# Kernel tuning notes

Hardware: AMD Instinct MI355X
Metric: run time of the kernel (lower is better)

Reference implementation:

```python
import jax, jax.numpy as jnp
import numpy as np

N, E, D_IN, D_HID, D_OUT = 100000, 1200000, 64, 64, 32


def setup_inputs() -> dict:
    key = jax.random.key(0)
    ks = jax.random.split(key, 8)
    x = jax.random.normal(ks[0], (N, D_IN), dtype=jnp.float32)
    edge_index = jax.random.randint(ks[1], (2, E), 0, N, dtype=jnp.int64)

    def w(k, din, dout):
        return jax.random.normal(k, (din, dout), dtype=jnp.float32) / jnp.sqrt(jnp.float32(din))

    return {
        "x": x,
        "edge_index": edge_index,
        # SAGEConv layer 1: lin_l (on aggregated neighbors, with bias) + lin_r (on self, no bias)
        "W_l1": w(ks[2], D_IN, D_HID),
        "W_r1": w(ks[3], D_IN, D_HID),
        "b1": jnp.zeros((D_HID,), jnp.float32),
        # SAGEConv layer 2
        "W_l2": w(ks[4], D_HID, D_OUT),
        "W_r2": w(ks[5], D_HID, D_OUT),
        "b2": jnp.zeros((D_OUT,), jnp.float32),
    }


def _sage_conv(x, src, dst, W_l, W_r, b, n_nodes):
    # mean-aggregate source features into destination nodes (PyG default 'mean')
    summed = jax.ops.segment_sum(x[src], dst, num_segments=n_nodes)          # [N, D]
    deg = jax.ops.segment_sum(jnp.ones(src.shape, x.dtype), dst, num_segments=n_nodes)
    mean = summed / jnp.maximum(deg, 1.0)[:, None]
    # out = lin_l(mean_neighbors) + lin_r(self)
    return mean @ W_l + b + x @ W_r


def reference(x, edge_index, W_l1, W_r1, b1, W_l2, W_r2, b2):
    src, dst = edge_index[0], edge_index[1]
    n_nodes = x.shape[0]
    h = _sage_conv(x, src, dst, W_l1, W_r1, b1, n_nodes)
    h = jax.nn.relu(h)
    out = _sage_conv(h, src, dst, W_l2, W_r2, b2, n_nodes)
    return out
```

## Files before the change

### kernel.cpp

```cpp
#include <hip/hip_runtime.h>
#include <hip/hip_bf16.h>


#define CHUNK 2048
#define BSHIFT 7
#define BCAP  2048

typedef __attribute__((ext_vector_type(8))) short bf8;
typedef __attribute__((ext_vector_type(4))) float f4;

__device__ __forceinline__ unsigned short f2b(float f) {
    unsigned u = __float_as_uint(f);
    u += 0x7FFF + ((u >> 16) & 1);
    return (unsigned short)(u >> 16);
}

__device__ __forceinline__ bf8 load8f(const float* __restrict__ p) {
    float4 u0 = *(const float4*)p, u1 = *(const float4*)(p + 4);
    bf8 r;
    r[0] = (short)f2b(u0.x); r[1] = (short)f2b(u0.y);
    r[2] = (short)f2b(u0.z); r[3] = (short)f2b(u0.w);
    r[4] = (short)f2b(u1.x); r[5] = (short)f2b(u1.y);
    r[6] = (short)f2b(u1.z); r[7] = (short)f2b(u1.w);
    return r;
}

__device__ __forceinline__ int edge_src(const int* ei, int E, int e, bool i64) {
    return i64 ? ei[2 * e] : ei[e];
}
__device__ __forceinline__ int edge_dst(const int* ei, int E, int e, bool i64) {
    return i64 ? ei[2 * E + 2 * e] : ei[E + e];
}

__global__ __launch_bounds__(256) void prep(
        const float* __restrict__ Wl1, const float* __restrict__ Wr1,
        const float* __restrict__ Wl2, const float* __restrict__ Wr2,
        const int* __restrict__ ei,
        unsigned short* __restrict__ Bp1, unsigned short* __restrict__ Bp2,
        int* __restrict__ flag, int* __restrict__ gcursor, int nbuck) {
    int blk = blockIdx.x, t = threadIdx.x;
    if (blk < 32) {
        int idx = blk * 256 + t;
        int j = idx & 7, lane = (idx >> 3) & 63, ks = (idx >> 9) & 1, ct = idx >> 10;
        int k = ks * 32 + ((lane >> 4) << 3) + j;
        int c = ct * 16 + (lane & 15);
        float v = (c < 64) ? Wl1[k * 64 + c] : Wr1[k * 64 + (c - 64)];
        Bp1[idx] = f2b(v);
    } else if (blk < 48) {
        int e = (blk - 32) * 256 + t;
        int j = e & 7, lane = (e >> 3) & 63, ks = (e >> 9) & 1, ct = e >> 10;
        int k = ks * 32 + ((lane >> 4) << 3) + j;
        int c = ct * 16 + (lane & 15);
        float v = (c < 32) ? Wl2[k * 32 + c] : Wr2[k * 32 + (c - 32)];
        Bp2[e] = f2b(v);
    } else {
        if (t == 0) *flag = 0;
        __syncthreads();
        int v = ei[2 * t + 1];
        if (v != 0) atomicOr(flag, 1);
        for (int b = t; b < nbuck; b += 256) gcursor[b] = b * BCAP;
    }
}

__global__ __launch_bounds__(256) void k_scatter(
        const int* __restrict__ ei, int E, const int* __restrict__ flag,
        int* __restrict__ gcursor, int* __restrict__ bucketed, int nbuck) {
    __shared__ int lhist[1024];
    __shared__ int wgbase[1024];
    int t = threadIdx.x;
#pragma unroll
    for (int i = 0; i < 4; ++i) lhist[t + 256 * i] = 0;
    __syncthreads();
    bool i64 = (flag[0] == 0);
    int base = blockIdx.x * CHUNK;
    int p[CHUNK / 256];
    int bk[CHUNK / 256];
#pragma unroll
    for (int i = 0; i < CHUNK / 256; ++i) {
        int e = base + i * 256 + t;
        if (e < E) {
            int s = edge_src(ei, E, e, i64);
            int d = edge_dst(ei, E, e, i64);
            p[i] = s | ((d & 127) << 24);
            bk[i] = d >> BSHIFT;
            atomicAdd(&lhist[bk[i]], 1);
        } else {
            bk[i] = -1;
        }
    }
    __syncthreads();
    for (int b = t; b < nbuck; b += 256) {
        int c = lhist[b];
        wgbase[b] = c ? atomicAdd(&gcursor[b], c) : 0;
        lhist[b] = 0;
    }
    __syncthreads();
#pragma unroll
    for (int i = 0; i < CHUNK / 256; ++i) {
        if (bk[i] >= 0) {
            int r = atomicAdd(&lhist[bk[i]], 1);
            bucketed[wgbase[bk[i]] + r] = p[i];
        }
    }
}

__global__ __launch_bounds__(256) void k_bfinal(
        const int* __restrict__ bucketed, const int* __restrict__ gcursor,
        int* __restrict__ rs, int* __restrict__ re,
        int* __restrict__ adj, int n) {
    __shared__ int ledge[BCAP];
    __shared__ unsigned short lrank[BCAP];
    __shared__ int ldeg[128];
    __shared__ int lstart[257];
    int t = threadIdx.x, b = blockIdx.x;
    int start = b * BCAP;
    int cnt = gcursor[b] - start;
    if (cnt > BCAP) cnt = BCAP;
    for (int i = t; i < cnt; i += 256) ledge[i] = bucketed[start + i];
    if (t < 128) ldeg[t] = 0;
    __syncthreads();
    for (int i = t; i < cnt; i += 256) {
        int dl = ((unsigned)ledge[i]) >> 24;
        lrank[i] = (unsigned short)atomicAdd(&ldeg[dl], 1);
    }
    __syncthreads();
    int v = (t < 128) ? ldeg[t] : 0;
    lstart[t + 1] = v;
    if (t == 0) lstart[0] = 0;
    __syncthreads();
    for (int off = 1; off < 256; off <<= 1) {
        int add = (t + 1 > off) ? lstart[t + 1 - off] : 0;
        __syncthreads();
        lstart[t + 1] += add;
        __syncthreads();
    }
    int node = b * 128 + t;
    if (t < 128 && node < n) {
        rs[node] = start + lstart[t];
        re[node] = start + lstart[t] + ldeg[t];
    }
    for (int i = t; i < cnt; i += 256) {
        int p = ledge[i];
        int dl = ((unsigned)p) >> 24;
        adj[start + lstart[dl] + lrank[i]] = p & 0xFFFFFF;
    }
}

__global__ __launch_bounds__(256) void mm1(
        const float* __restrict__ x, const unsigned short* __restrict__ Bp1,
        const float* __restrict__ b1, unsigned short* __restrict__ P1b,
        float* __restrict__ H, int n) {
    int lane = threadIdx.x & 63;
    int w = threadIdx.x >> 6;
    int rb = blockIdx.x * 64;
    int r15 = lane & 15, kg = lane >> 4;
    bf8 a[4][2];
#pragma unroll
    for (int rt = 0; rt < 4; ++rt) {
        int row = rb + rt * 16 + r15; if (row >= n) row = n - 1;
        const float* ap = x + (size_t)row * 64 + kg * 8;
        a[rt][0] = load8f(ap);
        a[rt][1] = load8f(ap + 32);
    }
    bf8 b[2][2];
#pragma unroll
    for (int ct2 = 0; ct2 < 2; ++ct2) {
        int ct = w * 2 + ct2;
#pragma unroll
        for (int ks = 0; ks < 2; ++ks)
            b[ct2][ks] = *(const bf8*)(Bp1 + ((size_t)(ct * 2 + ks) * 64 + lane) * 8);
    }
    f4 acc[4][2] = {};
#pragma unroll
    for (int rt = 0; rt < 4; ++rt)
#pragma unroll
        for (int ct2 = 0; ct2 < 2; ++ct2)
#pragma unroll
            for (int ks = 0; ks < 2; ++ks)
                acc[rt][ct2] = __builtin_amdgcn_mfma_f32_16x16x32_bf16(
                    a[rt][ks], b[ct2][ks], acc[rt][ct2], 0, 0, 0);
#pragma unroll
    for (int ct2 = 0; ct2 < 2; ++ct2) {
        int col = w * 32 + ct2 * 16 + r15;
        bool isH = col >= 64;
        float bias = isH ? b1[col - 64] : 0.f;
#pragma unroll
        for (int rt = 0; rt < 4; ++rt) {
            int row0 = rb + rt * 16 + kg * 4;
#pragma unroll
            for (int reg = 0; reg < 4; ++reg) {
                int row = row0 + reg;
                if (row < n) {
                    float val = acc[rt][ct2][reg];
                    if (isH) H[(size_t)row * 64 + (col - 64)] = val + bias;
                    else     P1b[(size_t)row * 64 + col] = f2b(val);
                }
            }
        }
    }
}

__global__ __launch_bounds__(256) void mm2(
        const unsigned short* __restrict__ hb, const unsigned short* __restrict__ Bp2,
        const float* __restrict__ b2, unsigned short* __restrict__ z2b,
        float* __restrict__ S2, int n) {
    int lane = threadIdx.x & 63;
    int w = threadIdx.x >> 6;
    int rb = blockIdx.x * 64;
    int r15 = lane & 15, kg = lane >> 4;
    bf8 a[4][2];
#pragma unroll
    for (int rt = 0; rt < 4; ++rt) {
        int row = rb + rt * 16 + r15; if (row >= n) row = n - 1;
        const unsigned short* ap = hb + (size_t)row * 64 + kg * 8;
        a[rt][0] = *(const bf8*)(ap);
        a[rt][1] = *(const bf8*)(ap + 32);
    }
    bf8 b[2];
#pragma unroll
    for (int ks = 0; ks < 2; ++ks)
        b[ks] = *(const bf8*)(Bp2 + ((size_t)(w * 2 + ks) * 64 + lane) * 8);
    f4 acc[4] = {};
#pragma unroll
    for (int rt = 0; rt < 4; ++rt)
#pragma unroll
        for (int ks = 0; ks < 2; ++ks)
            acc[rt] = __builtin_amdgcn_mfma_f32_16x16x32_bf16(
                a[rt][ks], b[ks], acc[rt], 0, 0, 0);
    int col = w * 16 + r15;
    bool isS = col >= 32;
    float bias = isS ? b2[col - 32] : 0.f;
#pragma unroll
    for (int rt = 0; rt < 4; ++rt) {
        int row0 = rb + rt * 16 + kg * 4;
#pragma unroll
        for (int reg = 0; reg < 4; ++reg) {
            int row = row0 + reg;
            if (row < n) {
                float val = acc[rt][reg];
                if (isS) S2[(size_t)row * 32 + (col - 32)] = val + bias;
                else     z2b[(size_t)row * 32 + col] = f2b(val);
            }
        }
    }
}

__global__ __launch_bounds__(256) void agg1(
        const unsigned short* __restrict__ P1b, const int* __restrict__ rs,
        const int* __restrict__ re, const int* __restrict__ adj,
        const float* __restrict__ H, unsigned short* __restrict__ hb, int n) {
    int w = threadIdx.x >> 6, lane = threadIdx.x & 63;
    int v = blockIdx.x * 4 + w;
    if (v >= n) return;
    int s0 = rs[v], s1 = re[v], last = s1 - 1;
    int e8 = lane >> 3, f8 = lane & 7;
    float acc[8] = {0.f, 0.f, 0.f, 0.f, 0.f, 0.f, 0.f, 0.f};
    const uint4* P4 = (const uint4*)P1b;
    for (int e = s0; e < s1; e += 16) {
#pragma unroll
        for (int u = 0; u < 2; ++u) {
            int ei = e + u * 8 + e8;
            int ec = ei > last ? last : ei;
            int src = adj[ec];
            uint4 q = P4[(size_t)src * 8 + f8];
            float m = (ei <= last) ? 1.f : 0.f;
            acc[0] = fmaf(m, __uint_as_float(q.x << 16), acc[0]);
            acc[1] = fmaf(m, __uint_as_float(q.x & 0xFFFF0000u), acc[1]);
            acc[2] = fmaf(m, __uint_as_float(q.y << 16), acc[2]);
            acc[3] = fmaf(m, __uint_as_float(q.y & 0xFFFF0000u), acc[3]);
            acc[4] = fmaf(m, __uint_as_float(q.z << 16), acc[4]);
            acc[5] = fmaf(m, __uint_as_float(q.z & 0xFFFF0000u), acc[5]);
            acc[6] = fmaf(m, __uint_as_float(q.w << 16), acc[6]);
            acc[7] = fmaf(m, __uint_as_float(q.w & 0xFFFF0000u), acc[7]);
        }
    }
#pragma unroll
    for (int off = 8; off <= 32; off <<= 1)
#pragma unroll
        for (int i = 0; i < 8; ++i) acc[i] += __shfl_xor(acc[i], off);
    if (lane < 8) {
        float inv = 1.f / fmaxf((float)(s1 - s0), 1.f);
        const float4* H4 = (const float4*)(H + (size_t)v * 64);
        float4 ha = H4[lane * 2], hc = H4[lane * 2 + 1];
        float h0 = fmaxf(fmaf(acc[0], inv, ha.x), 0.f);
        float h1 = fmaxf(fmaf(acc[1], inv, ha.y), 0.f);
        float h2 = fmaxf(fmaf(acc[2], inv, ha.z), 0.f);
        float h3 = fmaxf(fmaf(acc[3], inv, ha.w), 0.f);
        float h4 = fmaxf(fmaf(acc[4], inv, hc.x), 0.f);
        float h5 = fmaxf(fmaf(acc[5], inv, hc.y), 0.f);
        float h6 = fmaxf(fmaf(acc[6], inv, hc.z), 0.f);
        float h7 = fmaxf(fmaf(acc[7], inv, hc.w), 0.f);
        uint4 o;
        o.x = f2b(h0) | ((unsigned)f2b(h1) << 16);
        o.y = f2b(h2) | ((unsigned)f2b(h3) << 16);
        o.z = f2b(h4) | ((unsigned)f2b(h5) << 16);
        o.w = f2b(h6) | ((unsigned)f2b(h7) << 16);
        ((uint4*)hb)[(size_t)v * 8 + lane] = o;
    }
}

__global__ __launch_bounds__(256) void agg2(
        const unsigned short* __restrict__ z2b, const int* __restrict__ rs,
        const int* __restrict__ re, const int* __restrict__ adj,
        const float* __restrict__ S2, float* __restrict__ out, int n) {
    int w = threadIdx.x >> 6, lane = threadIdx.x & 63;
    int v = blockIdx.x * 4 + w;
    if (v >= n) return;
    int s0 = rs[v], s1 = re[v], last = s1 - 1;
    int e16 = lane >> 2, f4c = lane & 3;
    float acc[8] = {0.f, 0.f, 0.f, 0.f, 0.f, 0.f, 0.f, 0.f};
    const uint4* Z4 = (const uint4*)z2b;
    for (int e = s0; e < s1; e += 16) {
        int ei = e + e16;
        int ec = ei > last ? last : ei;
        int src = adj[ec];
        uint4 q = Z4[(size_t)src * 4 + f4c];
        float m = (ei <= last) ? 1.f : 0.f;
        acc[0] = fmaf(m, __uint_as_float(q.x << 16), acc[0]);
        acc[1] = fmaf(m, __uint_as_float(q.x & 0xFFFF0000u), acc[1]);
        acc[2] = fmaf(m, __uint_as_float(q.y << 16), acc[2]);
        acc[3] = fmaf(m, __uint_as_float(q.y & 0xFFFF0000u), acc[3]);
        acc[4] = fmaf(m, __uint_as_float(q.z << 16), acc[4]);
        acc[5] = fmaf(m, __uint_as_float(q.z & 0xFFFF0000u), acc[5]);
        acc[6] = fmaf(m, __uint_as_float(q.w << 16), acc[6]);
        acc[7] = fmaf(m, __uint_as_float(q.w & 0xFFFF0000u), acc[7]);
    }
#pragma unroll
    for (int off = 4; off <= 32; off <<= 1)
#pragma unroll
        for (int i = 0; i < 8; ++i) acc[i] += __shfl_xor(acc[i], off);
    if (lane < 4) {
        float inv = 1.f / fmaxf((float)(s1 - s0), 1.f);
        const float4* S4 = (const float4*)(S2 + (size_t)v * 32);
        float4 sa = S4[lane * 2], sb = S4[lane * 2 + 1];
        float4 oa, ob;
        oa.x = fmaf(acc[0], inv, sa.x);
        oa.y = fmaf(acc[1], inv, sa.y);
        oa.z = fmaf(acc[2], inv, sa.z);
        oa.w = fmaf(acc[3], inv, sa.w);
        ob.x = fmaf(acc[4], inv, sb.x);
        ob.y = fmaf(acc[5], inv, sb.y);
        ob.z = fmaf(acc[6], inv, sb.z);
        ob.w = fmaf(acc[7], inv, sb.w);
        ((float4*)(out + (size_t)v * 32))[lane * 2] = oa;
        ((float4*)(out + (size_t)v * 32))[lane * 2 + 1] = ob;
    }
}

extern "C" void kernel_launch(void* const* d_in, const int* in_sizes, int n_in,
                              void* d_out, int out_size, void* d_ws, size_t ws_size,
                              hipStream_t stream) {
    const float* x   = (const float*)d_in[0];
    const int*   ei  = (const int*)d_in[1];
    const float* Wl1 = (const float*)d_in[2];
    const float* Wr1 = (const float*)d_in[3];
    const float* b1  = (const float*)d_in[4];
    const float* Wl2 = (const float*)d_in[5];
    const float* Wr2 = (const float*)d_in[6];
    const float* b2  = (const float*)d_in[7];

    int N = in_sizes[0] / 64;
    int E = in_sizes[1] / 2;
    int nbuck = (N + 127) >> BSHIFT;

    char* ws = (char*)d_ws;
    size_t o = 0;
    auto alloc = [&](size_t bytes) -> char* {
        char* p = ws + o;
        o = (o + bytes + 255) & ~(size_t)255;
        return p;
    };
    int* flag     = (int*)alloc(4);
    int* gcursor  = (int*)alloc((size_t)nbuck * 4);
    int* rs       = (int*)alloc((size_t)N * 4);
    int* re       = (int*)alloc((size_t)N * 4);
    int* bucketed = (int*)alloc((size_t)nbuck * BCAP * 4);
    unsigned short* hbuf = (unsigned short*)alloc((size_t)N * 64 * 2);
    unsigned short* P1b  = (unsigned short*)alloc((size_t)N * 64 * 2);
    float* H      = (float*)alloc((size_t)N * 64 * 4);
    unsigned short* Bp1 = (unsigned short*)alloc(8192 * 2);
    unsigned short* Bp2 = (unsigned short*)alloc(4096 * 2);
    int* adj = bucketed;
    unsigned short* z2b = (unsigned short*)H;
    float* S2 = (float*)P1b;

    prep<<<49, 256, 0, stream>>>(Wl1, Wr1, Wl2, Wr2, ei, Bp1, Bp2, flag, gcursor, nbuck);

    int nwg = (E + CHUNK - 1) / CHUNK;
    k_scatter<<<nwg, 256, 0, stream>>>(ei, E, flag, gcursor, bucketed, nbuck);
    k_bfinal<<<nbuck, 256, 0, stream>>>(bucketed, gcursor, rs, re, adj, N);

    int nb64 = (N + 63) / 64;
    int nb4  = (N + 3) / 4;
    mm1<<<nb64, 256, 0, stream>>>(x, Bp1, b1, P1b, H, N);
    agg1<<<nb4, 256, 0, stream>>>(P1b, rs, re, adj, H, hbuf, N);
    mm2<<<nb64, 256, 0, stream>>>(hbuf, Bp2, b2, z2b, S2, N);
    agg2<<<nb4, 256, 0, stream>>>(z2b, rs, re, adj, S2, (float*)d_out, N);
}
```

Measured before the change: 157.5 us.

## Merge prep, edge scatter and first matmul into one kernel launch

```diff
diff --git a/kernel.cpp b/kernel.cpp
--- a/kernel.cpp
+++ b/kernel.cpp
@@ -14,6 +14,8 @@
     u += 0x7FFF + ((u >> 16) & 1);
     return (unsigned short)(u >> 16);
 }
+__device__ __forceinline__ float blo(unsigned u) { return __uint_as_float(u << 16); }
+__device__ __forceinline__ float bhi(unsigned u) { return __uint_as_float(u & 0xFFFF0000u); }
 
 __device__ __forceinline__ bf8 load8f(const float* __restrict__ p) {
     float4 u0 = *(const float4*)p, u1 = *(const float4*)(p + 4);
@@ -32,74 +34,118 @@
     return i64 ? ei[2 * E + 2 * e] : ei[E + e];
 }
 
-__global__ __launch_bounds__(256) void prep(
+__global__ __launch_bounds__(256) void mega1(
+        const int* __restrict__ ei, int E, int* __restrict__ gcursor,
+        int* __restrict__ bucketed, int nbuck, int nwg,
+        const float* __restrict__ x,
         const float* __restrict__ Wl1, const float* __restrict__ Wr1,
-        const float* __restrict__ Wl2, const float* __restrict__ Wr2,
-        const int* __restrict__ ei,
-        unsigned short* __restrict__ Bp1, unsigned short* __restrict__ Bp2,
-        int* __restrict__ flag, int* __restrict__ gcursor, int nbuck) {
-    int blk = blockIdx.x, t = threadIdx.x;
-    if (blk < 32) {
-        int idx = blk * 256 + t;
-        int j = idx & 7, lane = (idx >> 3) & 63, ks = (idx >> 9) & 1, ct = idx >> 10;
-        int k = ks * 32 + ((lane >> 4) << 3) + j;
-        int c = ct * 16 + (lane & 15);
-        float v = (c < 64) ? Wl1[k * 64 + c] : Wr1[k * 64 + (c - 64)];
-        Bp1[idx] = f2b(v);
-    } else if (blk < 48) {
-        int e = (blk - 32) * 256 + t;
-        int j = e & 7, lane = (e >> 3) & 63, ks = (e >> 9) & 1, ct = e >> 10;
-        int k = ks * 32 + ((lane >> 4) << 3) + j;
-        int c = ct * 16 + (lane & 15);
-        float v = (c < 32) ? Wl2[k * 32 + c] : Wr2[k * 32 + (c - 32)];
-        Bp2[e] = f2b(v);
-    } else {
-        if (t == 0) *flag = 0;
-        __syncthreads();
-        int v = ei[2 * t + 1];
-        if (v != 0) atomicOr(flag, 1);
-        for (int b = t; b < nbuck; b += 256) gcursor[b] = b * BCAP;
-    }
-}
-
-__global__ __launch_bounds__(256) void k_scatter(
-        const int* __restrict__ ei, int E, const int* __restrict__ flag,
-        int* __restrict__ gcursor, int* __restrict__ bucketed, int nbuck) {
+        const float* __restrict__ b1,
+        unsigned short* __restrict__ P1b, float* __restrict__ H, int n) {
     __shared__ int lhist[1024];
     __shared__ int wgbase[1024];
+    __shared__ int sflag;
     int t = threadIdx.x;
-#pragma unroll
-    for (int i = 0; i < 4; ++i) lhist[t + 256 * i] = 0;
-    __syncthreads();
-    bool i64 = (flag[0] == 0);
-    int base = blockIdx.x * CHUNK;
-    int p[CHUNK / 256];
-    int bk[CHUNK / 256];
-#pragma unroll
-    for (int i = 0; i < CHUNK / 256; ++i) {
-        int e = base + i * 256 + t;
-        if (e < E) {
-            int s = edge_src(ei, E, e, i64);
-            int d = edge_dst(ei, E, e, i64);
-            p[i] = s | ((d & 127) << 24);
-            bk[i] = d >> BSHIFT;
-            atomicAdd(&lhist[bk[i]], 1);
-        } else {
-            bk[i] = -1;
-        }
-    }
-    __syncthreads();
-    for (int b = t; b < nbuck; b += 256) {
-        int c = lhist[b];
-        wgbase[b] = c ? atomicAdd(&gcursor[b], c) : 0;
-        lhist[b] = 0;
-    }
-    __syncthreads();
-#pragma unroll
-    for (int i = 0; i < CHUNK / 256; ++i) {
-        if (bk[i] >= 0) {
-            int r = atomicAdd(&lhist[bk[i]], 1);
-            bucketed[wgbase[bk[i]] + r] = p[i];
+    if ((int)blockIdx.x < nwg) {
+        if (t == 0) sflag = 0;
+#pragma unroll
+        for (int i = 0; i < 4; ++i) lhist[t + 256 * i] = 0;
+        __syncthreads();
+        int base = blockIdx.x * CHUNK;
+        int myor = 0;
+#pragma unroll
+        for (int i = 0; i < CHUNK / 256; ++i) {
+            int e = base + i * 256 + t;
+            if (e < E) myor |= ei[2 * e + 1];
+        }
+        if (myor) atomicOr(&sflag, 1);
+        __syncthreads();
+        bool i64 = (sflag == 0);
+        int p[CHUNK / 256];
+        int bk[CHUNK / 256];
+#pragma unroll
+        for (int i = 0; i < CHUNK / 256; ++i) {
+            int e = base + i * 256 + t;
+            if (e < E) {
+                int s = edge_src(ei, E, e, i64);
+                int d = edge_dst(ei, E, e, i64);
+                p[i] = s | ((d & 127) << 24);
+                bk[i] = d >> BSHIFT;
+                atomicAdd(&lhist[bk[i]], 1);
+            } else {
+                bk[i] = -1;
+            }
+        }
+        __syncthreads();
+        for (int b = t; b < nbuck; b += 256) {
+            int c = lhist[b];
+            wgbase[b] = c ? atomicAdd(&gcursor[b], c) : 0;
+            lhist[b] = 0;
+        }
+        __syncthreads();
+#pragma unroll
+        for (int i = 0; i < CHUNK / 256; ++i) {
+            if (bk[i] >= 0) {
+                int r = atomicAdd(&lhist[bk[i]], 1);
+                int off = wgbase[bk[i]] + r;
+                if (off < BCAP) bucketed[(size_t)bk[i] * BCAP + off] = p[i];
+            }
+        }
+    } else {
+        int mb = blockIdx.x - nwg;
+        int lane = t & 63, w = t >> 6;
+        int rb = mb * 64;
+        int r15 = lane & 15, kg = lane >> 4;
+        bf8 a[4][2];
+#pragma unroll
+        for (int rt = 0; rt < 4; ++rt) {
+            int row = rb + rt * 16 + r15; if (row >= n) row = n - 1;
+            const float* ap = x + (size_t)row * 64 + kg * 8;
+            a[rt][0] = load8f(ap);
+            a[rt][1] = load8f(ap + 32);
+        }
+        bf8 b[2][2];
+#pragma unroll
+        for (int ct2 = 0; ct2 < 2; ++ct2) {
+            int c = (w * 2 + ct2) * 16 + r15;
+#pragma unroll
+            for (int ks = 0; ks < 2; ++ks) {
+                bf8 bv;
+#pragma unroll
+                for (int j = 0; j < 8; ++j) {
+                    int k = ks * 32 + kg * 8 + j;
+                    float wv = (c < 64) ? Wl1[k * 64 + c] : Wr1[k * 64 + (c - 64)];
+                    bv[j] = (short)f2b(wv);
+                }
+                b[ct2][ks] = bv;
+            }
+        }
+        f4 acc[4][2] = {};
+#pragma unroll
+        for (int rt = 0; rt < 4; ++rt)
+#pragma unroll
+            for (int ct2 = 0; ct2 < 2; ++ct2)
+#pragma unroll
+                for (int ks = 0; ks < 2; ++ks)
+                    acc[rt][ct2] = __builtin_amdgcn_mfma_f32_16x16x32_bf16(
+                        a[rt][ks], b[ct2][ks], acc[rt][ct2], 0, 0, 0);
+#pragma unroll
+        for (int ct2 = 0; ct2 < 2; ++ct2) {
+            int col = (w * 2 + ct2) * 16 + r15;
+            bool isH = col >= 64;
+            float bias = isH ? b1[col - 64] : 0.f;
+#pragma unroll
+            for (int rt = 0; rt < 4; ++rt) {
+                int row0 = rb + rt * 16 + kg * 4;
+#pragma unroll
+                for (int reg = 0; reg < 4; ++reg) {
+                    int row = row0 + reg;
+                    if (row < n) {
+                        float val = acc[rt][ct2][reg];
+                        if (isH) H[(size_t)row * 64 + (col - 64)] = val + bias;
+                        else     P1b[(size_t)row * 64 + col] = f2b(val);
+                    }
+                }
+            }
         }
     }
 }
@@ -114,7 +160,7 @@
     __shared__ int lstart[257];
     int t = threadIdx.x, b = blockIdx.x;
     int start = b * BCAP;
-    int cnt = gcursor[b] - start;
+    int cnt = gcursor[b];
     if (cnt > BCAP) cnt = BCAP;
     for (int i = t; i < cnt; i += 256) ledge[i] = bucketed[start + i];
     if (t < 128) ldeg[t] = 0;
@@ -143,105 +189,6 @@
         int p = ledge[i];
         int dl = ((unsigned)p) >> 24;
         adj[start + lstart[dl] + lrank[i]] = p & 0xFFFFFF;
-    }
-}
-
-__global__ __launch_bounds__(256) void mm1(
-        const float* __restrict__ x, const unsigned short* __restrict__ Bp1,
-        const float* __restrict__ b1, unsigned short* __restrict__ P1b,
-        float* __restrict__ H, int n) {
-    int lane = threadIdx.x & 63;
-    int w = threadIdx.x >> 6;
-    int rb = blockIdx.x * 64;
-    int r15 = lane & 15, kg = lane >> 4;
-    bf8 a[4][2];
-#pragma unroll
-    for (int rt = 0; rt < 4; ++rt) {
-        int row = rb + rt * 16 + r15; if (row >= n) row = n - 1;
-        const float* ap = x + (size_t)row * 64 + kg * 8;
-        a[rt][0] = load8f(ap);
-        a[rt][1] = load8f(ap + 32);
-    }
-    bf8 b[2][2];
-#pragma unroll
-    for (int ct2 = 0; ct2 < 2; ++ct2) {
-        int ct = w * 2 + ct2;
-#pragma unroll
-        for (int ks = 0; ks < 2; ++ks)
-            b[ct2][ks] = *(const bf8*)(Bp1 + ((size_t)(ct * 2 + ks) * 64 + lane) * 8);
-    }
-    f4 acc[4][2] = {};
-#pragma unroll
-    for (int rt = 0; rt < 4; ++rt)
-#pragma unroll
-        for (int ct2 = 0; ct2 < 2; ++ct2)
-#pragma unroll
-            for (int ks = 0; ks < 2; ++ks)
-                acc[rt][ct2] = __builtin_amdgcn_mfma_f32_16x16x32_bf16(
-                    a[rt][ks], b[ct2][ks], acc[rt][ct2], 0, 0, 0);
-#pragma unroll
-    for (int ct2 = 0; ct2 < 2; ++ct2) {
-        int col = w * 32 + ct2 * 16 + r15;
-        bool isH = col >= 64;
-        float bias = isH ? b1[col - 64] : 0.f;
-#pragma unroll
-        for (int rt = 0; rt < 4; ++rt) {
-            int row0 = rb + rt * 16 + kg * 4;
-#pragma unroll
-            for (int reg = 0; reg < 4; ++reg) {
-                int row = row0 + reg;
-                if (row < n) {
-                    float val = acc[rt][ct2][reg];
-                    if (isH) H[(size_t)row * 64 + (col - 64)] = val + bias;
-                    else     P1b[(size_t)row * 64 + col] = f2b(val);
-                }
-            }
-        }
-    }
-}
-
-__global__ __launch_bounds__(256) void mm2(
-        const unsigned short* __restrict__ hb, const unsigned short* __restrict__ Bp2,
-        const float* __restrict__ b2, unsigned short* __restrict__ z2b,
-        float* __restrict__ S2, int n) {
-    int lane = threadIdx.x & 63;
-    int w = threadIdx.x >> 6;
-    int rb = blockIdx.x * 64;
-    int r15 = lane & 15, kg = lane >> 4;
-    bf8 a[4][2];
-#pragma unroll
-    for (int rt = 0; rt < 4; ++rt) {
-        int row = rb + rt * 16 + r15; if (row >= n) row = n - 1;
-        const unsigned short* ap = hb + (size_t)row * 64 + kg * 8;
-        a[rt][0] = *(const bf8*)(ap);
-        a[rt][1] = *(const bf8*)(ap + 32);
-    }
-    bf8 b[2];
-#pragma unroll
-    for (int ks = 0; ks < 2; ++ks)
-        b[ks] = *(const bf8*)(Bp2 + ((size_t)(w * 2 + ks) * 64 + lane) * 8);
-    f4 acc[4] = {};
-#pragma unroll
-    for (int rt = 0; rt < 4; ++rt)
-#pragma unroll
-        for (int ks = 0; ks < 2; ++ks)
-            acc[rt] = __builtin_amdgcn_mfma_f32_16x16x32_bf16(
-                a[rt][ks], b[ks], acc[rt], 0, 0, 0);
-    int col = w * 16 + r15;
-    bool isS = col >= 32;
-    float bias = isS ? b2[col - 32] : 0.f;
-#pragma unroll
-    for (int rt = 0; rt < 4; ++rt) {
-        int row0 = rb + rt * 16 + kg * 4;
-#pragma unroll
-        for (int reg = 0; reg < 4; ++reg) {
-            int row = row0 + reg;
-            if (row < n) {
-                float val = acc[rt][reg];
-                if (isS) S2[(size_t)row * 32 + (col - 32)] = val + bias;
-                else     z2b[(size_t)row * 32 + col] = f2b(val);
-            }
-        }
     }
 }
 
@@ -264,14 +211,14 @@
             int src = adj[ec];
             uint4 q = P4[(size_t)src * 8 + f8];
             float m = (ei <= last) ? 1.f : 0.f;
-            acc[0] = fmaf(m, __uint_as_float(q.x << 16), acc[0]);
-            acc[1] = fmaf(m, __uint_as_float(q.x & 0xFFFF0000u), acc[1]);
-            acc[2] = fmaf(m, __uint_as_float(q.y << 16), acc[2]);
-            acc[3] = fmaf(m, __uint_as_float(q.y & 0xFFFF0000u), acc[3]);
-            acc[4] = fmaf(m, __uint_as_float(q.z << 16), acc[4]);
-            acc[5] = fmaf(m, __uint_as_float(q.z & 0xFFFF0000u), acc[5]);
-            acc[6] = fmaf(m, __uint_as_float(q.w << 16), acc[6]);
-            acc[7] = fmaf(m, __uint_as_float(q.w & 0xFFFF0000u), acc[7]);
+            acc[0] = fmaf(m, blo(q.x), acc[0]);
+            acc[1] = fmaf(m, bhi(q.x), acc[1]);
+            acc[2] = fmaf(m, blo(q.y), acc[2]);
+            acc[3] = fmaf(m, bhi(q.y), acc[3]);
+            acc[4] = fmaf(m, blo(q.z), acc[4]);
+            acc[5] = fmaf(m, bhi(q.z), acc[5]);
+            acc[6] = fmaf(m, blo(q.w), acc[6]);
+            acc[7] = fmaf(m, bhi(q.w), acc[7]);
         }
     }
 #pragma unroll
@@ -299,31 +246,80 @@
     }
 }
 
+__global__ __launch_bounds__(256) void mm2(
+        const unsigned short* __restrict__ hb,
+        const float* __restrict__ Wl2, const float* __restrict__ Wr2,
+        const float* __restrict__ b2, unsigned short* __restrict__ zs, int n) {
+    int lane = threadIdx.x & 63;
+    int w = threadIdx.x >> 6;
+    int rb = blockIdx.x * 64;
+    int r15 = lane & 15, kg = lane >> 4;
+    bf8 a[4][2];
+#pragma unroll
+    for (int rt = 0; rt < 4; ++rt) {
+        int row = rb + rt * 16 + r15; if (row >= n) row = n - 1;
+        const unsigned short* ap = hb + (size_t)row * 64 + kg * 8;
+        a[rt][0] = *(const bf8*)(ap);
+        a[rt][1] = *(const bf8*)(ap + 32);
+    }
+    int c = w * 16 + r15;
+    bf8 b[2];
+#pragma unroll
+    for (int ks = 0; ks < 2; ++ks) {
+        bf8 bv;
+#pragma unroll
+        for (int j = 0; j < 8; ++j) {
+            int k = ks * 32 + kg * 8 + j;
+            float wv = (c < 32) ? Wl2[k * 32 + c] : Wr2[k * 32 + (c - 32)];
+            bv[j] = (short)f2b(wv);
+        }
+        b[ks] = bv;
+    }
+    f4 acc[4] = {};
+#pragma unroll
+    for (int rt = 0; rt < 4; ++rt)
+#pragma unroll
+        for (int ks = 0; ks < 2; ++ks)
+            acc[rt] = __builtin_amdgcn_mfma_f32_16x16x32_bf16(
+                a[rt][ks], b[ks], acc[rt], 0, 0, 0);
+    bool isS = c >= 32;
+    float bias = isS ? b2[c - 32] : 0.f;
+#pragma unroll
+    for (int rt = 0; rt < 4; ++rt) {
+        int row0 = rb + rt * 16 + kg * 4;
+#pragma unroll
+        for (int reg = 0; reg < 4; ++reg) {
+            int row = row0 + reg;
+            if (row < n) zs[(size_t)row * 64 + c] = f2b(acc[rt][reg] + bias);
+        }
+    }
+}
+
 __global__ __launch_bounds__(256) void agg2(
-        const unsigned short* __restrict__ z2b, const int* __restrict__ rs,
+        const unsigned short* __restrict__ zs, const int* __restrict__ rs,
         const int* __restrict__ re, const int* __restrict__ adj,
-        const float* __restrict__ S2, float* __restrict__ out, int n) {
+        float* __restrict__ out, int n) {
     int w = threadIdx.x >> 6, lane = threadIdx.x & 63;
     int v = blockIdx.x * 4 + w;
     if (v >= n) return;
     int s0 = rs[v], s1 = re[v], last = s1 - 1;
     int e16 = lane >> 2, f4c = lane & 3;
     float acc[8] = {0.f, 0.f, 0.f, 0.f, 0.f, 0.f, 0.f, 0.f};
-    const uint4* Z4 = (const uint4*)z2b;
+    const uint4* Z4 = (const uint4*)zs;
     for (int e = s0; e < s1; e += 16) {
         int ei = e + e16;
         int ec = ei > last ? last : ei;
         int src = adj[ec];
-        uint4 q = Z4[(size_t)src * 4 + f4c];
+        uint4 q = Z4[(size_t)src * 8 + f4c];
         float m = (ei <= last) ? 1.f : 0.f;
-        acc[0] = fmaf(m, __uint_as_float(q.x << 16), acc[0]);
-        acc[1] = fmaf(m, __uint_as_float(q.x & 0xFFFF0000u), acc[1]);
-        acc[2] = fmaf(m, __uint_as_float(q.y << 16), acc[2]);
-        acc[3] = fmaf(m, __uint_as_float(q.y & 0xFFFF0000u), acc[3]);
-        acc[4] = fmaf(m, __uint_as_float(q.z << 16), acc[4]);
-        acc[5] = fmaf(m, __uint_as_float(q.z & 0xFFFF0000u), acc[5]);
-        acc[6] = fmaf(m, __uint_as_float(q.w << 16), acc[6]);
-        acc[7] = fmaf(m, __uint_as_float(q.w & 0xFFFF0000u), acc[7]);
+        acc[0] = fmaf(m, blo(q.x), acc[0]);
+        acc[1] = fmaf(m, bhi(q.x), acc[1]);
+        acc[2] = fmaf(m, blo(q.y), acc[2]);
+        acc[3] = fmaf(m, bhi(q.y), acc[3]);
+        acc[4] = fmaf(m, blo(q.z), acc[4]);
+        acc[5] = fmaf(m, bhi(q.z), acc[5]);
+        acc[6] = fmaf(m, blo(q.w), acc[6]);
+        acc[7] = fmaf(m, bhi(q.w), acc[7]);
     }
 #pragma unroll
     for (int off = 4; off <= 32; off <<= 1)
@@ -331,19 +327,21 @@
         for (int i = 0; i < 8; ++i) acc[i] += __shfl_xor(acc[i], off);
     if (lane < 4) {
         float inv = 1.f / fmaxf((float)(s1 - s0), 1.f);
-        const float4* S4 = (const float4*)(S2 + (size_t)v * 32);
-        float4 sa = S4[lane * 2], sb = S4[lane * 2 + 1];
-        float4 oa, ob;
-        oa.x = fmaf(acc[0], inv, sa.x);
-        oa.y = fmaf(acc[1], inv, sa.y);
-        oa.z = fmaf(acc[2], inv, sa.z);
-        oa.w = fmaf(acc[3], inv, sa.w);
-        ob.x = fmaf(acc[4], inv, sb.x);
-        ob.y = fmaf(acc[5], inv, sb.y);
-        ob.z = fmaf(acc[6], inv, sb.z);
-        ob.w = fmaf(acc[7], inv, sb.w);
-        ((float4*)(out + (size_t)v * 32))[lane * 2] = oa;
-        ((float4*)(out + (size_t)v * 32))[lane * 2 + 1] = ob;
+        const uint4* srow = (const uint4*)(zs + (size_t)v * 64 + 32);
+        uint4 u0 = srow[lane];
+        float sv[8] = {blo(u0.x), bhi(u0.x), blo(u0.y), bhi(u0.y),
+                       blo(u0.z), bhi(u0.z), blo(u0.w), bhi(u0.w)};
+        float4 o0, o1;
+        o0.x = fmaf(acc[0], inv, sv[0]);
+        o0.y = fmaf(acc[1], inv, sv[1]);
+        o0.z = fmaf(acc[2], inv, sv[2]);
+        o0.w = fmaf(acc[3], inv, sv[3]);
+        o1.x = fmaf(acc[4], inv, sv[4]);
+        o1.y = fmaf(acc[5], inv, sv[5]);
+        o1.z = fmaf(acc[6], inv, sv[6]);
+        o1.w = fmaf(acc[7], inv, sv[7]);
+        ((float4*)(out + (size_t)v * 32))[lane * 2] = o0;
+        ((float4*)(out + (size_t)v * 32))[lane * 2 + 1] = o1;
     }
 }
 
@@ -370,30 +368,25 @@
         o = (o + bytes + 255) & ~(size_t)255;
         return p;
     };
-    int* flag     = (int*)alloc(4);
     int* gcursor  = (int*)alloc((size_t)nbuck * 4);
     int* rs       = (int*)alloc((size_t)N * 4);
     int* re       = (int*)alloc((size_t)N * 4);
     int* bucketed = (int*)alloc((size_t)nbuck * BCAP * 4);
+    unsigned short* P1b  = (unsigned short*)alloc((size_t)N * 64 * 2);
     unsigned short* hbuf = (unsigned short*)alloc((size_t)N * 64 * 2);
-    unsigned short* P1b  = (unsigned short*)alloc((size_t)N * 64 * 2);
     float* H      = (float*)alloc((size_t)N * 64 * 4);
-    unsigned short* Bp1 = (unsigned short*)alloc(8192 * 2);
-    unsigned short* Bp2 = (unsigned short*)alloc(4096 * 2);
     int* adj = bucketed;
-    unsigned short* z2b = (unsigned short*)H;
-    float* S2 = (float*)P1b;
-
-    prep<<<49, 256, 0, stream>>>(Wl1, Wr1, Wl2, Wr2, ei, Bp1, Bp2, flag, gcursor, nbuck);
-
-    int nwg = (E + CHUNK - 1) / CHUNK;
-    k_scatter<<<nwg, 256, 0, stream>>>(ei, E, flag, gcursor, bucketed, nbuck);
-    k_bfinal<<<nbuck, 256, 0, stream>>>(bucketed, gcursor, rs, re, adj, N);
-
+    unsigned short* zs = (unsigned short*)H;
+
+    hipMemsetAsync(gcursor, 0, (size_t)nbuck * 4, stream);
+
+    int nwg  = (E + CHUNK - 1) / CHUNK;
     int nb64 = (N + 63) / 64;
     int nb4  = (N + 3) / 4;
-    mm1<<<nb64, 256, 0, stream>>>(x, Bp1, b1, P1b, H, N);
+    mega1<<<nwg + nb64, 256, 0, stream>>>(ei, E, gcursor, bucketed, nbuck, nwg,
+                                          x, Wl1, Wr1, b1, P1b, H, N);
+    k_bfinal<<<nbuck, 256, 0, stream>>>(bucketed, gcursor, rs, re, adj, N);
     agg1<<<nb4, 256, 0, stream>>>(P1b, rs, re, adj, H, hbuf, N);
-    mm2<<<nb64, 256, 0, stream>>>(hbuf, Bp2, b2, z2b, S2, N);
-    agg2<<<nb4, 256, 0, stream>>>(z2b, rs, re, adj, S2, (float*)d_out, N);
-}
+    mm2<<<nb64, 256, 0, stream>>>(hbuf, Wl2, Wr2, b2, zs, N);
+    agg2<<<nb4, 256, 0, stream>>>(zs, rs, re, adj, (float*)d_out, N);
+}
```

Result: no change. 155.9 us (-1.0%).
